# Kernel optimization log

Measured on AMD Instinct MI355X. Metric: run time of the kernel, lower is better.

The kernel has to match this reference:

```python
import jax, jax.numpy as jnp
import numpy as np

MAX_SP = 180.0
MAX_TP = 365.0
NUM_HEADS = 4
HEAD_SIZE = 32
ALL_HEAD = NUM_HEADS * HEAD_SIZE  # 128
HIDDEN = 256
FIRE_H = 32


def _fire(dist, c, w1, w2, max_dist):
    # dist: (B,N); w1: (FIRE_H,1); w2: (1,FIRE_H)
    d = dist[..., None].astype(jnp.float32)
    c = jnp.maximum(c, 0.0)
    d = jnp.log(c * d + 1.0) / jnp.log(c * max_dist + 1.0)
    h = jax.nn.silu(d @ w1.T)          # (B,N,FIRE_H)
    return (h @ w2.T)[..., 0]          # (B,N)


def setup_inputs() -> dict:
    key = jax.random.key(0)
    ks = jax.random.split(key, 20)
    B, S, N, C = 8, 256, 128, 64
    inp = {
        "source_ids": jax.random.randint(ks[0], (B, S, N), 0, 2),
        "source_cluster_labels": jax.random.randint(ks[1], (B, N), 0, C),
        "in_cluster_spatial_dist": jax.random.uniform(ks[2], (B, N), dtype=jnp.float32),
        "in_cluster_temporal_dist": jax.random.uniform(ks[3], (B, N), dtype=jnp.float32),
        "num_clusters": C,
        # FIRE spatial params
        "c_sp": jnp.asarray(100.0, jnp.float32),
        "sp_w1": 0.1 * jax.random.normal(ks[4], (FIRE_H, 1), jnp.float32),
        "sp_w2": 0.1 * jax.random.normal(ks[5], (1, FIRE_H), jnp.float32),
        # FIRE temporal params
        "c_tp": jnp.asarray(100.0, jnp.float32),
        "tp_w1": 0.1 * jax.random.normal(ks[6], (FIRE_H, 1), jnp.float32),
        "tp_w2": 0.1 * jax.random.normal(ks[7], (1, FIRE_H), jnp.float32),
        # attention_weights: Linear(1, num_heads)
        "attn_w": 0.1 * jax.random.normal(ks[8], (NUM_HEADS,), jnp.float32),
        "attn_b": 0.1 * jax.random.normal(ks[9], (NUM_HEADS,), jnp.float32),
        # value: Linear(1, all_head_size)
        "val_w": 0.1 * jax.random.normal(ks[10], (ALL_HEAD,), jnp.float32),
        "val_b": 0.1 * jax.random.normal(ks[11], (ALL_HEAD,), jnp.float32),
        # ffn: Linear(all_head_size, hidden)
        "ffn_w": 0.05 * jax.random.normal(ks[12], (HIDDEN, ALL_HEAD), jnp.float32),
        "ffn_b": 0.05 * jax.random.normal(ks[13], (HIDDEN,), jnp.float32),
    }
    return inp


def reference(source_ids, source_cluster_labels, in_cluster_spatial_dist,
              in_cluster_temporal_dist, num_clusters,
              c_sp, sp_w1, sp_w2, c_tp, tp_w1, tp_w2,
              attn_w, attn_b, val_w, val_b, ffn_w, ffn_b):
    B, S, N = source_ids.shape
    C = num_clusters
    # FIRE distance biases over source sites: (B,N)
    bias = (_fire(in_cluster_spatial_dist, c_sp, sp_w1, sp_w2, MAX_SP)
            + _fire(in_cluster_temporal_dist, c_tp, tp_w1, tp_w2, MAX_TP))
    x = source_ids.astype(jnp.float32)                 # (B,S,N)
    attn_logits = x[..., None] * attn_w + attn_b       # (B,S,N,H)
    v = (x[..., None] * val_w + val_b).reshape(B, S, N, NUM_HEADS, HEAD_SIZE)
    attn_logits = attn_logits + bias[:, None, :, None]
    member = jax.nn.one_hot(source_cluster_labels, C, dtype=jnp.float32)  # (B,N,C)
    non_member = (1.0 - member)[:, None, :, None, :] * -1e9               # (B,1,N,1,C)
    masked = attn_logits[..., None] + non_member       # (B,S,N,H,C)
    probs = jnp.nan_to_num(jax.nn.softmax(masked, axis=2))
    # pool members per cluster: (B,S,C,H,head_size)
    pooled = jnp.einsum('bsnhc,bsnhd->bschd', probs, v).reshape(B, S, C, ALL_HEAD)
    out = pooled @ ffn_w.T + ffn_b                     # (B,S,C,HIDDEN)
    has_member = jnp.any(member > 0, axis=1)           # (B,C)
    return out * has_member[:, None, :, None].astype(out.dtype)
```

## Files before the change

### kernel.cpp

```cpp
#include <hip/hip_runtime.h>
#include <hip/hip_bf16.h>

#define NB 8
#define NS 256
#define NN 128
#define NC 64
#define NH 4
#define AH 128
#define HID 256
#define FH 32

typedef float f32x4 __attribute__((ext_vector_type(4)));


__global__ __launch_bounds__(256) void prep_kernel(
    const int* __restrict__ labels,
    const float* __restrict__ sp_d, const float* __restrict__ tp_d,
    const float* __restrict__ c_sp_p, const float* __restrict__ sp_w1, const float* __restrict__ sp_w2,
    const float* __restrict__ c_tp_p, const float* __restrict__ tp_w1, const float* __restrict__ tp_w2,
    const float* __restrict__ attn_w,
    const float* __restrict__ val_w, const float* __restrict__ val_b,
    const float* __restrict__ ffn_w, const float* __restrict__ ffn_b,
    float* __restrict__ ws)
{
    const int blk = blockIdx.x;
    const int t = threadIdx.x;

    if (blk < NB) {
        const int b = blk;
        __shared__ float sE[NN];
        __shared__ int   sLab[NN];
        __shared__ float sW1s[FH], sW2s[FH], sW1t[FH], sW2t[FH];

        if (t < FH) {
            sW1s[t] = sp_w1[t]; sW2s[t] = sp_w2[t];
            sW1t[t] = tp_w1[t]; sW2t[t] = tp_w2[t];
        }
        __syncthreads();

        if (t < NN) {
            const float csp = fmaxf(c_sp_p[0], 0.0f);
            const float ctp = fmaxf(c_tp_p[0], 0.0f);
            const float dsp = sp_d[b * NN + t];
            const float dtp = tp_d[b * NN + t];
            const float dns = __logf(fmaf(csp, dsp, 1.0f)) / __logf(fmaf(csp, 180.0f, 1.0f));
            const float dnt = __logf(fmaf(ctp, dtp, 1.0f)) / __logf(fmaf(ctp, 365.0f, 1.0f));
            float bias_sp = 0.f, bias_tp = 0.f;
            #pragma unroll
            for (int j = 0; j < FH; ++j) {
                const float zs = dns * sW1s[j];
                bias_sp += (zs / (1.0f + __expf(-zs))) * sW2s[j];
                const float zt = dnt * sW1t[j];
                bias_tp += (zt / (1.0f + __expf(-zt))) * sW2t[j];
            }
            const float e = __expf(bias_sp + bias_tp);
            sE[t] = e;
            sLab[t] = labels[b * NN + t];
            ws[b * NN + t] = e;
        }
        __syncthreads();

        {
            const int c = t >> 2, q = t & 3;
            float sum = 0.f;
            #pragma unroll
            for (int i = 0; i < 32; ++i) {
                const int n = (i << 2) | q;
                sum += (sLab[n] == c) ? sE[n] : 0.f;
            }
            sum += __shfl_xor(sum, 1);
            sum += __shfl_xor(sum, 2);
            if (q == 0) ws[1024 + b * NC + c] = sum;
        }
    } else {
        __shared__ float sVw[AH], sVb[AH];
        if (t < AH) { sVw[t] = val_w[t]; sVb[t] = val_b[t]; }
        __syncthreads();

        const int o = t;
        const float4* fr = reinterpret_cast<const float4*>(ffn_w + o * AH);
        float c0 = ffn_b[o];
        float w[NH] = {0.f, 0.f, 0.f, 0.f};
        #pragma unroll
        for (int k4 = 0; k4 < AH / 4; ++k4) {
            const float4 f = fr[k4];
            const int k = k4 * 4;
            const int h = k >> 5;
            c0 = fmaf(f.x, sVb[k], fmaf(f.y, sVb[k + 1], fmaf(f.z, sVb[k + 2], fmaf(f.w, sVb[k + 3], c0))));
            w[h] = fmaf(f.x, sVw[k], fmaf(f.y, sVw[k + 1], fmaf(f.z, sVw[k + 2], fmaf(f.w, sVw[k + 3], w[h]))));
        }
        ws[1536 + o] = c0;
        float4 wv = make_float4(w[0], w[1], w[2], w[3]);
        *reinterpret_cast<float4*>(ws + 1792 + o * NH) = wv;
        if (t < NH) ws[2816 + t] = __expf(attn_w[t]);
    }
}

__global__ __launch_bounds__(256) void out_kernel(
    const int* __restrict__ src,
    const int* __restrict__ labels,
    const float* __restrict__ ws,
    float* __restrict__ out)
{
    __shared__ float sEx[NN];
    __shared__ int   sLab[NN];
    __shared__ float sP1[NC][NH];
    __shared__ float sHm[NC];

    const int blk = blockIdx.x;
    const int b = blk >> 8;
    const int t = threadIdx.x;

    if (t < NN) {
        const float e = ws[b * NN + t];
        const int   x = src[(size_t)blk * NN + t];
        sLab[t] = labels[b * NN + t];
        sEx[t]  = x ? e : 0.f;
    }
    __syncthreads();

    {
        const int c = t >> 2, q = t & 3;
        float bs = 0.f;
        #pragma unroll
        for (int i = 0; i < 32; ++i) {
            const int n = (i << 2) | q;
            bs += (sLab[n] == c) ? sEx[n] : 0.f;
        }
        bs += __shfl_xor(bs, 1);
        bs += __shfl_xor(bs, 2);
        const float T = ws[1024 + b * NC + c];
        float p1 = 0.f, hm = 0.f;
        if (T > 0.f) {
            hm = 1.f;
            const float ew = ws[2816 + q];
            p1 = (bs * ew) / ((T - bs) + bs * ew);
        }
        sP1[c][q] = p1;
        if (q == 0) sHm[c] = hm;
    }
    __syncthreads();

    const int o0 = (t & 63) * 4;
    const int crow = t >> 6;
    float c0[4], w0[4], w1[4], w2[4], w3[4];
    #pragma unroll
    for (int i = 0; i < 4; ++i) {
        c0[i] = ws[1536 + o0 + i];
        const float* wp = ws + 1792 + (size_t)(o0 + i) * NH;
        w0[i] = wp[0]; w1[i] = wp[1]; w2[i] = wp[2]; w3[i] = wp[3];
    }
    float* orow = out + (size_t)blk * (NC * HID);
    #pragma unroll
    for (int ci = 0; ci < 16; ++ci) {
        const int c = ci * 4 + crow;
        const float p0 = sP1[c][0], p1v = sP1[c][1], p2 = sP1[c][2], p3 = sP1[c][3];
        const float hm = sHm[c];
        f32x4 val;
        #pragma unroll
        for (int i = 0; i < 4; ++i) {
            float v = c0[i];
            v = fmaf(p0,  w0[i], v);
            v = fmaf(p1v, w1[i], v);
            v = fmaf(p2,  w2[i], v);
            val[i] = fmaf(p3, w3[i], v) * hm;
        }
        __builtin_nontemporal_store(val, reinterpret_cast<f32x4*>(orow + (size_t)c * HID + o0));
    }
}

extern "C" void kernel_launch(void* const* d_in, const int* in_sizes, int n_in,
                              void* d_out, int out_size, void* d_ws, size_t ws_size,
                              hipStream_t stream) {
    const int*   src    = (const int*)d_in[0];
    const int*   labels = (const int*)d_in[1];
    const float* sp_d   = (const float*)d_in[2];
    const float* tp_d   = (const float*)d_in[3];
    const float* c_sp   = (const float*)d_in[5];
    const float* sp_w1  = (const float*)d_in[6];
    const float* sp_w2  = (const float*)d_in[7];
    const float* c_tp   = (const float*)d_in[8];
    const float* tp_w1  = (const float*)d_in[9];
    const float* tp_w2  = (const float*)d_in[10];
    const float* attn_w = (const float*)d_in[11];
    const float* val_w  = (const float*)d_in[13];
    const float* val_b  = (const float*)d_in[14];
    const float* ffn_w  = (const float*)d_in[15];
    const float* ffn_b  = (const float*)d_in[16];
    float* ws = (float*)d_ws;
    float* out = (float*)d_out;

    prep_kernel<<<NB + 1, 256, 0, stream>>>(labels, sp_d, tp_d, c_sp, sp_w1, sp_w2,
                                            c_tp, tp_w1, tp_w2, attn_w, val_w, val_b,
                                            ffn_w, ffn_b, ws);
    out_kernel<<<NB * NS, 256, 0, stream>>>(src, labels, ws, out);
}
```

Before: 38.95 us.

## Fuse FIRE bias into output kernel and process two sequence rows per block

Moves the per-batch FIRE bias, exp and cluster total computation from the prep kernel into the output kernel, leaving a single-block fold kernel for the FFN weight folding. Each output block now handles two s rows, sharing the bias computation and the weight register loads across them, and launches half as many blocks. The bias (a 32-term silu loop per site) is recomputed redundantly in every block, and the larger per-block store work may reduce latency hiding. The output write (about 16 MB) still dominates the runtime.

```diff
diff --git a/kernel.cpp b/kernel.cpp
--- a/kernel.cpp
+++ b/kernel.cpp
@@ -13,159 +13,134 @@
 typedef float f32x4 __attribute__((ext_vector_type(4)));
 
 
-__global__ __launch_bounds__(256) void prep_kernel(
+__global__ __launch_bounds__(256) void fold_kernel(
+    const float* __restrict__ val_w, const float* __restrict__ val_b,
+    const float* __restrict__ ffn_w, const float* __restrict__ ffn_b,
+    float* __restrict__ ws)
+{
+    __shared__ float sVw[AH], sVb[AH];
+    const int t = threadIdx.x;
+    if (t < AH) { sVw[t] = val_w[t]; sVb[t] = val_b[t]; }
+    __syncthreads();
+
+    const int o = t;
+    const float4* fr = reinterpret_cast<const float4*>(ffn_w + o * AH);
+    float c0 = ffn_b[o];
+    float w[NH] = {0.f, 0.f, 0.f, 0.f};
+    #pragma unroll
+    for (int k4 = 0; k4 < AH / 4; ++k4) {
+        const float4 f = fr[k4];
+        const int k = k4 * 4;
+        const int h = k >> 5;
+        c0  = fmaf(f.x, sVb[k], fmaf(f.y, sVb[k+1], fmaf(f.z, sVb[k+2], fmaf(f.w, sVb[k+3], c0))));
+        w[h] = fmaf(f.x, sVw[k], fmaf(f.y, sVw[k+1], fmaf(f.z, sVw[k+2], fmaf(f.w, sVw[k+3], w[h]))));
+    }
+    ws[1536 + o] = c0;
+    *reinterpret_cast<float4*>(ws + 1792 + o * NH) = make_float4(w[0], w[1], w[2], w[3]);
+}
+
+__global__ __launch_bounds__(256) void out_kernel(
+    const int* __restrict__ src,
     const int* __restrict__ labels,
     const float* __restrict__ sp_d, const float* __restrict__ tp_d,
     const float* __restrict__ c_sp_p, const float* __restrict__ sp_w1, const float* __restrict__ sp_w2,
     const float* __restrict__ c_tp_p, const float* __restrict__ tp_w1, const float* __restrict__ tp_w2,
     const float* __restrict__ attn_w,
-    const float* __restrict__ val_w, const float* __restrict__ val_b,
-    const float* __restrict__ ffn_w, const float* __restrict__ ffn_b,
-    float* __restrict__ ws)
-{
-    const int blk = blockIdx.x;
-    const int t = threadIdx.x;
-
-    if (blk < NB) {
-        const int b = blk;
-        __shared__ float sE[NN];
-        __shared__ int   sLab[NN];
-        __shared__ float sW1s[FH], sW2s[FH], sW1t[FH], sW2t[FH];
-
-        if (t < FH) {
-            sW1s[t] = sp_w1[t]; sW2s[t] = sp_w2[t];
-            sW1t[t] = tp_w1[t]; sW2t[t] = tp_w2[t];
-        }
-        __syncthreads();
-
-        if (t < NN) {
-            const float csp = fmaxf(c_sp_p[0], 0.0f);
-            const float ctp = fmaxf(c_tp_p[0], 0.0f);
-            const float dsp = sp_d[b * NN + t];
-            const float dtp = tp_d[b * NN + t];
-            const float dns = __logf(fmaf(csp, dsp, 1.0f)) / __logf(fmaf(csp, 180.0f, 1.0f));
-            const float dnt = __logf(fmaf(ctp, dtp, 1.0f)) / __logf(fmaf(ctp, 365.0f, 1.0f));
-            float bias_sp = 0.f, bias_tp = 0.f;
-            #pragma unroll
-            for (int j = 0; j < FH; ++j) {
-                const float zs = dns * sW1s[j];
-                bias_sp += (zs / (1.0f + __expf(-zs))) * sW2s[j];
-                const float zt = dnt * sW1t[j];
-                bias_tp += (zt / (1.0f + __expf(-zt))) * sW2t[j];
-            }
-            const float e = __expf(bias_sp + bias_tp);
-            sE[t] = e;
-            sLab[t] = labels[b * NN + t];
-            ws[b * NN + t] = e;
-        }
-        __syncthreads();
-
-        {
-            const int c = t >> 2, q = t & 3;
-            float sum = 0.f;
-            #pragma unroll
-            for (int i = 0; i < 32; ++i) {
-                const int n = (i << 2) | q;
-                sum += (sLab[n] == c) ? sE[n] : 0.f;
-            }
-            sum += __shfl_xor(sum, 1);
-            sum += __shfl_xor(sum, 2);
-            if (q == 0) ws[1024 + b * NC + c] = sum;
-        }
-    } else {
-        __shared__ float sVw[AH], sVb[AH];
-        if (t < AH) { sVw[t] = val_w[t]; sVb[t] = val_b[t]; }
-        __syncthreads();
-
-        const int o = t;
-        const float4* fr = reinterpret_cast<const float4*>(ffn_w + o * AH);
-        float c0 = ffn_b[o];
-        float w[NH] = {0.f, 0.f, 0.f, 0.f};
-        #pragma unroll
-        for (int k4 = 0; k4 < AH / 4; ++k4) {
-            const float4 f = fr[k4];
-            const int k = k4 * 4;
-            const int h = k >> 5;
-            c0 = fmaf(f.x, sVb[k], fmaf(f.y, sVb[k + 1], fmaf(f.z, sVb[k + 2], fmaf(f.w, sVb[k + 3], c0))));
-            w[h] = fmaf(f.x, sVw[k], fmaf(f.y, sVw[k + 1], fmaf(f.z, sVw[k + 2], fmaf(f.w, sVw[k + 3], w[h]))));
-        }
-        ws[1536 + o] = c0;
-        float4 wv = make_float4(w[0], w[1], w[2], w[3]);
-        *reinterpret_cast<float4*>(ws + 1792 + o * NH) = wv;
-        if (t < NH) ws[2816 + t] = __expf(attn_w[t]);
-    }
-}
-
-__global__ __launch_bounds__(256) void out_kernel(
-    const int* __restrict__ src,
-    const int* __restrict__ labels,
     const float* __restrict__ ws,
     float* __restrict__ out)
 {
-    __shared__ float sEx[NN];
+    __shared__ float sE[NN], sEx0[NN], sEx1[NN];
     __shared__ int   sLab[NN];
-    __shared__ float sP1[NC][NH];
+    __shared__ float sPa[NC][NH], sPb[NC][NH];
     __shared__ float sHm[NC];
 
     const int blk = blockIdx.x;
-    const int b = blk >> 8;
-    const int t = threadIdx.x;
+    const int b  = blk >> 7;
+    const int s0 = (blk & 127) * 2;
+    const int t  = threadIdx.x;
+
+    const int o0 = (t & 63) * 4;
+    const int crow = t >> 6;
+    const f32x4 c0v = *reinterpret_cast<const f32x4*>(ws + 1536 + o0);
+    f32x4 wrow[4];
+    #pragma unroll
+    for (int i = 0; i < 4; ++i)
+        wrow[i] = *reinterpret_cast<const f32x4*>(ws + 1792 + (size_t)(o0 + i) * NH);
 
     if (t < NN) {
-        const float e = ws[b * NN + t];
-        const int   x = src[(size_t)blk * NN + t];
-        sLab[t] = labels[b * NN + t];
-        sEx[t]  = x ? e : 0.f;
+        const float csp = fmaxf(c_sp_p[0], 0.0f);
+        const float ctp = fmaxf(c_tp_p[0], 0.0f);
+        const float dsp = sp_d[b * NN + t];
+        const float dtp = tp_d[b * NN + t];
+        const int   lab = labels[b * NN + t];
+        const int   x0  = src[((size_t)(b * NS + s0))     * NN + t];
+        const int   x1  = src[((size_t)(b * NS + s0 + 1)) * NN + t];
+        const float dns = __logf(fmaf(csp, dsp, 1.0f)) / __logf(fmaf(csp, 180.0f, 1.0f));
+        const float dnt = __logf(fmaf(ctp, dtp, 1.0f)) / __logf(fmaf(ctp, 365.0f, 1.0f));
+        float bias_sp = 0.f, bias_tp = 0.f;
+        #pragma unroll
+        for (int j = 0; j < FH; ++j) {
+            const float zs = dns * sp_w1[j];
+            bias_sp += (zs / (1.0f + __expf(-zs))) * sp_w2[j];
+            const float zt = dnt * tp_w1[j];
+            bias_tp += (zt / (1.0f + __expf(-zt))) * tp_w2[j];
+        }
+        const float e = __expf(bias_sp + bias_tp);
+        sE[t]   = e;
+        sLab[t] = lab;
+        sEx0[t] = x0 ? e : 0.f;
+        sEx1[t] = x1 ? e : 0.f;
     }
     __syncthreads();
 
     {
         const int c = t >> 2, q = t & 3;
-        float bs = 0.f;
+        float tS = 0.f, b0 = 0.f, b1 = 0.f;
         #pragma unroll
         for (int i = 0; i < 32; ++i) {
             const int n = (i << 2) | q;
-            bs += (sLab[n] == c) ? sEx[n] : 0.f;
+            const bool m = (sLab[n] == c);
+            tS += m ? sE[n]   : 0.f;
+            b0 += m ? sEx0[n] : 0.f;
+            b1 += m ? sEx1[n] : 0.f;
         }
-        bs += __shfl_xor(bs, 1);
-        bs += __shfl_xor(bs, 2);
-        const float T = ws[1024 + b * NC + c];
-        float p1 = 0.f, hm = 0.f;
-        if (T > 0.f) {
+        tS += __shfl_xor(tS, 1); tS += __shfl_xor(tS, 2);
+        b0 += __shfl_xor(b0, 1); b0 += __shfl_xor(b0, 2);
+        b1 += __shfl_xor(b1, 1); b1 += __shfl_xor(b1, 2);
+        float p0 = 0.f, p1 = 0.f, hm = 0.f;
+        if (tS > 0.f) {
             hm = 1.f;
-            const float ew = ws[2816 + q];
-            p1 = (bs * ew) / ((T - bs) + bs * ew);
+            const float ew = __expf(attn_w[q]);
+            p0 = (b0 * ew) / ((tS - b0) + b0 * ew);
+            p1 = (b1 * ew) / ((tS - b1) + b1 * ew);
         }
-        sP1[c][q] = p1;
+        sPa[c][q] = p0;
+        sPb[c][q] = p1;
         if (q == 0) sHm[c] = hm;
     }
     __syncthreads();
 
-    const int o0 = (t & 63) * 4;
-    const int crow = t >> 6;
-    float c0[4], w0[4], w1[4], w2[4], w3[4];
+    float* orow0 = out + ((size_t)(b * NS + s0)) * (NC * HID);
     #pragma unroll
-    for (int i = 0; i < 4; ++i) {
-        c0[i] = ws[1536 + o0 + i];
-        const float* wp = ws + 1792 + (size_t)(o0 + i) * NH;
-        w0[i] = wp[0]; w1[i] = wp[1]; w2[i] = wp[2]; w3[i] = wp[3];
-    }
-    float* orow = out + (size_t)blk * (NC * HID);
-    #pragma unroll
-    for (int ci = 0; ci < 16; ++ci) {
-        const int c = ci * 4 + crow;
-        const float p0 = sP1[c][0], p1v = sP1[c][1], p2 = sP1[c][2], p3 = sP1[c][3];
-        const float hm = sHm[c];
-        f32x4 val;
+    for (int ss = 0; ss < 2; ++ss) {
+        float* orow = orow0 + (size_t)ss * (NC * HID);
         #pragma unroll
-        for (int i = 0; i < 4; ++i) {
-            float v = c0[i];
-            v = fmaf(p0,  w0[i], v);
-            v = fmaf(p1v, w1[i], v);
-            v = fmaf(p2,  w2[i], v);
-            val[i] = fmaf(p3, w3[i], v) * hm;
+        for (int ci = 0; ci < 16; ++ci) {
+            const int c = ci * 4 + crow;
+            const float* P = ss ? sPb[c] : sPa[c];
+            const float p0 = P[0], p1 = P[1], p2 = P[2], p3 = P[3];
+            const float hm = sHm[c];
+            f32x4 val;
+            #pragma unroll
+            for (int i = 0; i < 4; ++i) {
+                float v = c0v[i];
+                v = fmaf(p0, wrow[i][0], v);
+                v = fmaf(p1, wrow[i][1], v);
+                v = fmaf(p2, wrow[i][2], v);
+                val[i] = fmaf(p3, wrow[i][3], v) * hm;
+            }
+            __builtin_nontemporal_store(val, reinterpret_cast<f32x4*>(orow + (size_t)c * HID + o0));
         }
-        __builtin_nontemporal_store(val, reinterpret_cast<f32x4*>(orow + (size_t)c * HID + o0));
     }
 }
 
@@ -190,8 +165,9 @@
     float* ws = (float*)d_ws;
     float* out = (float*)d_out;
 
-    prep_kernel<<<NB + 1, 256, 0, stream>>>(labels, sp_d, tp_d, c_sp, sp_w1, sp_w2,
-                                            c_tp, tp_w1, tp_w2, attn_w, val_w, val_b,
-                                            ffn_w, ffn_b, ws);
-    out_kernel<<<NB * NS, 256, 0, stream>>>(src, labels, ws, out);
+    fold_kernel<<<1, 256, 0, stream>>>(val_w, val_b, ffn_w, ffn_b, ws);
+    out_kernel<<<NB * NS / 2, 256, 0, stream>>>(src, labels, sp_d, tp_d,
+                                                c_sp, sp_w1, sp_w2,
+                                                c_tp, tp_w1, tp_w2,
+                                                attn_w, ws, out);
 }
```

Measured after the change: 39.88 us. +2.4%, slower.
